# Performance work log

Measured on AMD Instinct MI355X. Metric: run time of the kernel, lower is better.

The kernel has to match this reference:

```python
import jax, jax.numpy as jnp
import numpy as np

B, S, H = 2, 2048, 1024
NH, HD = 16, 64
SCALE = HD ** -0.5


def setup_inputs() -> dict:
    key = jax.random.key(0)
    k1, k2, k3, k4 = jax.random.split(key, 4)
    hidden_states = jax.random.normal(k1, (B, S, H), dtype=jnp.float32)
    attention_mask = jax.random.randint(k2, (B, S), 0, 2, dtype=jnp.int32)
    # xavier-uniform-ish init scale
    w_qkv = jax.random.normal(k3, (3 * H, H), dtype=jnp.float32) * (2.0 / (H + 3 * H)) ** 0.5
    w_out = jax.random.normal(k4, (H, H), dtype=jnp.float32) * (1.0 / H) ** 0.5
    return {"hidden_states": hidden_states, "attention_mask": attention_mask,
            "w_qkv": w_qkv, "w_out": w_out}


def reference(hidden_states, attention_mask, w_qkv, w_out):
    b, s, _ = hidden_states.shape
    qkv = hidden_states @ w_qkv.T                      # [B,S,3H]
    q, k, v = jnp.split(qkv, 3, axis=-1)
    # [B,S,H] -> [B,NH,S,HD]
    reshape = lambda x: x.reshape(b, s, NH, HD).transpose(0, 2, 1, 3)
    q, k, v = reshape(q), reshape(k), reshape(v)
    scores = jnp.einsum('bhqd,bhkd->bhqk', q, k) * SCALE   # [B,NH,S,S]
    mask = attention_mask[:, None, None, :] == 0           # [B,1,1,S]
    scores = jnp.where(mask, -jnp.inf, scores)
    attn = jax.nn.softmax(scores, axis=-1)                 # dropout p: eval mode -> identity
    out = jnp.einsum('bhqk,bhkd->bhqd', attn, v)           # [B,NH,S,HD]
    out = out.transpose(0, 2, 1, 3).reshape(b, s, H)
    return out @ w_out.T
```

## Files before the change

### kernel.cpp

```cpp
#include <hip/hip_runtime.h>
#include <string.h>


typedef __bf16    bf16x8 __attribute__((ext_vector_type(8)));
typedef _Float16  f16x4  __attribute__((ext_vector_type(4)));
typedef _Float16  f16x2  __attribute__((ext_vector_type(2)));
typedef float     f32x4  __attribute__((ext_vector_type(4)));

#define NTOK   4096
#define HDIM   1024
#define SEQ    2048
#define NHEAD  16
#define F2SHIFT 4.0f
#define QSCALE  0.18033688f
#define LSTRIDE 68

__device__ __forceinline__ float bf2f(unsigned short u) {
    union { unsigned int i; float f; } x;
    x.i = ((unsigned int)u) << 16;
    return x.f;
}
__device__ __forceinline__ unsigned short f2bf(float f) {
    union { __bf16 h; unsigned short u; } x;
    x.h = (__bf16)f;
    return x.u;
}
__device__ __forceinline__ unsigned short f2h(float f) {
    union { _Float16 h; unsigned short u; } x;
    x.h = (_Float16)f;
    return x.u;
}
__device__ __forceinline__ f16x2 pkrtz(float a, float b) {
    union { __fp16 __attribute__((ext_vector_type(2))) i; f16x2 o; } x;
    x.i = __builtin_amdgcn_cvt_pkrtz(a, b);
    return x.o;
}

__device__ __forceinline__ int detect_f32(const unsigned short* hs) {
    unsigned int idx = (threadIdx.x & 63) * 4096u;
    float f = bf2f(hs[idx]);
    return __any(!(fabsf(f) < 1e4f));
}

typedef const __attribute__((address_space(1))) unsigned int* gptr_u32;
typedef __attribute__((address_space(3))) unsigned int* lptr_u32;

__device__ __forceinline__ void async16(const unsigned short* g, unsigned short* l) {
    __builtin_amdgcn_global_load_lds((gptr_u32)g, (lptr_u32)l, 16, 0, 0);
}

__global__ void convert3_kernel(const void* __restrict__ s0, const void* __restrict__ s1,
                                const void* __restrict__ s2, unsigned short* __restrict__ dst) {
    const int isf32 = detect_f32((const unsigned short*)s0);
    if (!isf32) return;
    int g = blockIdx.x * blockDim.x + threadIdx.x;
    const int stride = gridDim.x * blockDim.x;
    for (; g < 1048576; g += stride) {
        int i = g * 8;
        const void* src; int off;
        if (i < 4194304)      { src = s0; off = i; }
        else if (i < 7340032) { src = s1; off = i - 4194304; }
        else                  { src = s2; off = i - 7340032; }
        const float* s = (const float*)src + off;
        unsigned short o[8];
#pragma unroll
        for (int j = 0; j < 8; j++) o[j] = f2bf(s[j]);
        *(uint4*)(dst + i) = *(const uint4*)o;
    }
}

__global__ __launch_bounds__(256) void gemm_qkv(
    const unsigned short* __restrict__ Xc, const unsigned short* __restrict__ Wc,
    const unsigned short* __restrict__ Xraw, const unsigned short* __restrict__ Wraw,
    unsigned short* __restrict__ q_out, unsigned short* __restrict__ k_out,
    unsigned short* __restrict__ v_out) {
    const int K = 1024;
    __shared__ __align__(16) unsigned short Xs0[128 * 32];
    __shared__ __align__(16) unsigned short Xs1[128 * 32];
    __shared__ __align__(16) unsigned short Ws0[128 * 32];
    __shared__ __align__(16) unsigned short Ws1[128 * 32];

    const int isf32 = detect_f32(Xraw);
    const unsigned short* X = isf32 ? Xc : Xraw;
    const unsigned short* W = isf32 ? Wc : Wraw;

    const int t = threadIdx.x;
    const int w = t >> 6, lane = t & 63, quad = lane >> 4, lr = lane & 15;
    const int wrow = (w >> 1) * 64, wcol = (w & 1) * 64;

    const int hid = blockIdx.x;
    const int xcd = hid & 7, r = hid >> 3;
    const int by = xcd * 4 + r / 24;
    const int bx = r % 24;
    const int m0 = by * 128, n0 = bx * 128;
    const bool vblk = (n0 >= 2048);

    f32x4 acc[4][4];
#pragma unroll
    for (int mi = 0; mi < 4; mi++)
#pragma unroll
        for (int ni = 0; ni < 4; ni++) acc[mi][ni] = (f32x4){0.f, 0.f, 0.f, 0.f};

    const int srow = w * 32 + (lane >> 2);
    const int scol = (lane & 3) * 8;
    const unsigned short* xg = X + (size_t)(m0 + srow) * K + scol;
    const unsigned short* wg = W + (size_t)(n0 + srow) * K + scol;
    unsigned short* xl0 = &Xs0[w * 1024];
    unsigned short* xl1 = &Xs1[w * 1024];
    unsigned short* wl0 = &Ws0[w * 1024];
    unsigned short* wl1 = &Ws1[w * 1024];

    async16(xg, xl0);
    async16(xg + 16 * K, xl0 + 512);
    async16(wg, wl0);
    async16(wg + 16 * K, wl0 + 512);

#define QKV_COMPUTE(Xh, Wh)                                                            \
    {                                                                                  \
        bf16x8 af[4], bfr[4];                                                          \
        _Pragma("unroll")                                                              \
        for (int mi = 0; mi < 4; mi++)                                                 \
            af[mi] = *(const bf16x8*)&Xh[(wrow + mi * 16 + lr) * 32 + quad * 8];       \
        _Pragma("unroll")                                                              \
        for (int ni = 0; ni < 4; ni++)                                                 \
            bfr[ni] = *(const bf16x8*)&Wh[(wcol + ni * 16 + lr) * 32 + quad * 8];      \
        __builtin_amdgcn_s_setprio(1);                                                 \
        if (!vblk) {                                                                   \
            _Pragma("unroll")                                                          \
            for (int mi = 0; mi < 4; mi++)                                             \
                _Pragma("unroll")                                                      \
                for (int ni = 0; ni < 4; ni++)                                         \
                    acc[mi][ni] = __builtin_amdgcn_mfma_f32_16x16x32_bf16(             \
                        af[mi], bfr[ni], acc[mi][ni], 0, 0, 0);                        \
        } else {                                                                       \
            _Pragma("unroll")                                                          \
            for (int mi = 0; mi < 4; mi++)                                             \
                _Pragma("unroll")                                                      \
                for (int ni = 0; ni < 4; ni++)                                         \
                    acc[mi][ni] = __builtin_amdgcn_mfma_f32_16x16x32_bf16(             \
                        bfr[ni], af[mi], acc[mi][ni], 0, 0, 0);                        \
        }                                                                              \
        __builtin_amdgcn_s_setprio(0);                                                 \
    }

    for (int k0 = 0; k0 < K; k0 += 64) {
        __syncthreads();
        async16(xg + k0 + 32, xl1);
        async16(xg + k0 + 32 + 16 * K, xl1 + 512);
        async16(wg + k0 + 32, wl1);
        async16(wg + k0 + 32 + 16 * K, wl1 + 512);
        QKV_COMPUTE(Xs0, Ws0);

        __syncthreads();
        if (k0 + 64 < K) {
            async16(xg + k0 + 64, xl0);
            async16(xg + k0 + 64 + 16 * K, xl0 + 512);
            async16(wg + k0 + 64, wl0);
            async16(wg + k0 + 64 + 16 * K, wl0 + 512);
        }
        QKV_COMPUTE(Xs1, Ws1);
    }
#undef QKV_COMPUTE

    if (!vblk) {
#pragma unroll
        for (int mi = 0; mi < 4; mi++)
#pragma unroll
            for (int ni = 0; ni < 4; ni++)
#pragma unroll
                for (int rr = 0; rr < 4; rr++) {
                    int mrow = m0 + wrow + mi * 16 + quad * 4 + rr;
                    int j = n0 + wcol + ni * 16 + lr;
                    float val = acc[mi][ni][rr];
                    int which = j >> 10, rem = j & 1023;
                    int nh = rem >> 6, hd = rem & 63;
                    int b = mrow >> 11, s = mrow & 2047;
                    size_t dst = ((size_t)(b * NHEAD + nh) * SEQ + s) * 64 + hd;
                    if (which == 0) q_out[dst] = f2bf(val * QSCALE);
                    else            k_out[dst] = f2bf(val);
                }
    } else {
#pragma unroll
        for (int mi = 0; mi < 4; mi++)
#pragma unroll
            for (int ni = 0; ni < 4; ni++)
#pragma unroll
                for (int rr = 0; rr < 4; rr++) {
                    int n = n0 + wcol + ni * 16 + quad * 4 + rr;
                    int m = m0 + wrow + mi * 16 + lr;
                    float val = acc[mi][ni][rr];
                    int rem = n & 1023;
                    int nh = rem >> 6, hd = rem & 63;
                    int b = m >> 11, s = m & 2047;
                    size_t dst = ((size_t)(b * NHEAD + nh) * 64 + hd) * SEQ + s;
                    v_out[dst] = f2h(val);
                }
    }
}

__global__ __launch_bounds__(256) void gemm_out(
    const unsigned short* __restrict__ X, const unsigned short* __restrict__ Wc,
    const unsigned short* __restrict__ Wraw,
    void* __restrict__ d_out, const unsigned short* __restrict__ hs_raw) {
    const int K = 1024, N = 1024;
    __shared__ __align__(16) unsigned short Xs0[64 * 32];
    __shared__ __align__(16) unsigned short Xs1[64 * 32];
    __shared__ __align__(16) unsigned short Ws0[128 * 32];
    __shared__ __align__(16) unsigned short Ws1[128 * 32];

    const int isf32 = detect_f32(hs_raw);
    const unsigned short* W = isf32 ? Wc : Wraw;

    const int t = threadIdx.x;
    const int w = t >> 6, lane = t & 63, quad = lane >> 4, lr = lane & 15;
    const int wrow = (w >> 1) * 32, wcol = (w & 1) * 64;
    const int m0 = blockIdx.y * 64, n0 = blockIdx.x * 128;

    f32x4 acc[2][4];
#pragma unroll
    for (int mi = 0; mi < 2; mi++)
#pragma unroll
        for (int ni = 0; ni < 4; ni++) acc[mi][ni] = (f32x4){0.f, 0.f, 0.f, 0.f};

    const int sxrow = w * 16 + (lane >> 2);
    const int swrow = w * 32 + (lane >> 2);
    const int scol = (lane & 3) * 8;
    const unsigned short* xg = X + (size_t)(m0 + sxrow) * K + scol;
    const unsigned short* wg = W + (size_t)(n0 + swrow) * K + scol;
    unsigned short* xl0 = &Xs0[w * 512];
    unsigned short* xl1 = &Xs1[w * 512];
    unsigned short* wl0 = &Ws0[w * 1024];
    unsigned short* wl1 = &Ws1[w * 1024];

    async16(xg, xl0);
    async16(wg, wl0);
    async16(wg + 16 * K, wl0 + 512);

#define OUT_COMPUTE(Xh, Wh)                                                            \
    {                                                                                  \
        bf16x8 af[2], bfr[4];                                                          \
        _Pragma("unroll")                                                              \
        for (int mi = 0; mi < 2; mi++)                                                 \
            af[mi] = *(const bf16x8*)&Xh[(wrow + mi * 16 + lr) * 32 + quad * 8];       \
        _Pragma("unroll")                                                              \
        for (int ni = 0; ni < 4; ni++)                                                 \
            bfr[ni] = *(const bf16x8*)&Wh[(wcol + ni * 16 + lr) * 32 + quad * 8];      \
        __builtin_amdgcn_s_setprio(1);                                                 \
        _Pragma("unroll")                                                              \
        for (int mi = 0; mi < 2; mi++)                                                 \
            _Pragma("unroll")                                                          \
            for (int ni = 0; ni < 4; ni++)                                             \
                acc[mi][ni] = __builtin_amdgcn_mfma_f32_16x16x32_bf16(                 \
                    af[mi], bfr[ni], acc[mi][ni], 0, 0, 0);                            \
        __builtin_amdgcn_s_setprio(0);                                                 \
    }

    for (int k0 = 0; k0 < K; k0 += 64) {
        __syncthreads();
        async16(xg + k0 + 32, xl1);
        async16(wg + k0 + 32, wl1);
        async16(wg + k0 + 32 + 16 * K, wl1 + 512);
        OUT_COMPUTE(Xs0, Ws0);

        __syncthreads();
        if (k0 + 64 < K) {
            async16(xg + k0 + 64, xl0);
            async16(wg + k0 + 64, wl0);
            async16(wg + k0 + 64 + 16 * K, wl0 + 512);
        }
        OUT_COMPUTE(Xs1, Ws1);
    }
#undef OUT_COMPUTE

#pragma unroll
    for (int mi = 0; mi < 2; mi++)
#pragma unroll
        for (int ni = 0; ni < 4; ni++)
#pragma unroll
            for (int rr = 0; rr < 4; rr++) {
                int mrow = m0 + wrow + mi * 16 + quad * 4 + rr;
                int j = n0 + wcol + ni * 16 + lr;
                float val = acc[mi][ni][rr];
                size_t dst = (size_t)mrow * N + j;
                if (isf32) ((float*)d_out)[dst] = val;
                else ((unsigned short*)d_out)[dst] = f2bf(val);
            }
}

__global__ __launch_bounds__(256, 2) void flash_attn_v12(
    const unsigned short* __restrict__ q, const unsigned short* __restrict__ k,
    const unsigned short* __restrict__ vt, const int* __restrict__ mask,
    unsigned short* __restrict__ attn_out) {
    __shared__ __align__(16) unsigned short Ks[128 * LSTRIDE];
    __shared__ __align__(16) unsigned short Vt0[64 * LSTRIDE];
    __shared__ __align__(16) unsigned short Vt1[64 * LSTRIDE];
    __shared__ __align__(16) float Msk[136];

    const int t = threadIdx.x;
    const int w = t >> 6, lane = t & 63, quad = lane >> 4, lr = lane & 15;
    const int bh = blockIdx.x, b = bh >> 4, h = bh & 15;
    const int q0 = blockIdx.y * 128;

    const unsigned short* qb = q + (size_t)bh * SEQ * 64;
    const unsigned short* kb = k + (size_t)bh * SEQ * 64;
    const unsigned short* vtb = vt + (size_t)bh * 64 * SEQ;
    const int* mb = mask + b * SEQ;

    bf16x8 qf[2][2];
#pragma unroll
    for (int qg = 0; qg < 2; qg++) {
        const unsigned short* qrow = qb + (size_t)(q0 + w * 32 + qg * 16 + lr) * 64 + quad * 8;
        qf[qg][0] = *(const bf16x8*)qrow;
        qf[qg][1] = *(const bf16x8*)(qrow + 32);
    }

    f32x4 oacc[2][4];
#pragma unroll
    for (int qg = 0; qg < 2; qg++)
#pragma unroll
        for (int dt = 0; dt < 4; dt++) oacc[qg][dt] = (f32x4){0.f, 0.f, 0.f, 0.f};
    float l_st[2] = {0.f, 0.f};

    const int sr = t >> 2;
    const int sc = (t & 3) * 16;

    for (int kk0 = 0; kk0 < SEQ; kk0 += 128) {
        const uint4* kp0 = (const uint4*)(kb + (size_t)(kk0 + sr) * 64 + sc);
        const uint4* kp1 = (const uint4*)(kb + (size_t)(kk0 + 64 + sr) * 64 + sc);
        const uint4* vp0 = (const uint4*)(vtb + (size_t)sr * SEQ + kk0 + sc);
        const uint4* vp1 = (const uint4*)(vtb + (size_t)sr * SEQ + kk0 + 64 + sc);
        uint4 k0a = kp0[0], k0b = kp0[1];
        uint4 k1a = kp1[0], k1b = kp1[1];
        uint4 v0a = vp0[0], v0b = vp0[1];
        uint4 v1a = vp1[0], v1b = vp1[1];
        float mval = 0.f;
        if (t < 128) mval = (mb[kk0 + t] == 0) ? -1e30f : -F2SHIFT;

        __syncthreads();
        *(uint4*)&Ks[sr * LSTRIDE + sc] = k0a;
        *(uint4*)&Ks[sr * LSTRIDE + sc + 8] = k0b;
        *(uint4*)&Ks[(64 + sr) * LSTRIDE + sc] = k1a;
        *(uint4*)&Ks[(64 + sr) * LSTRIDE + sc + 8] = k1b;
        *(uint4*)&Vt0[sr * LSTRIDE + sc] = v0a;
        *(uint4*)&Vt0[sr * LSTRIDE + sc + 8] = v0b;
        *(uint4*)&Vt1[sr * LSTRIDE + sc] = v1a;
        *(uint4*)&Vt1[sr * LSTRIDE + sc + 8] = v1b;
        if (t < 128) Msk[t] = mval;
        __syncthreads();

        __builtin_amdgcn_s_setprio(1);
#pragma unroll
        for (int mt = 0; mt < 8; mt++) {
            bf16x8 a1h0 = *(bf16x8*)&Ks[(mt * 16 + lr) * LSTRIDE + quad * 8];
            bf16x8 a1h1 = *(bf16x8*)&Ks[(mt * 16 + lr) * LSTRIDE + 32 + quad * 8];
            const unsigned short* vb_ = (mt < 4) ? Vt0 : Vt1;
            const int mcol = (mt & 3) * 16;
            f16x4 a2[4];
#pragma unroll
            for (int dt = 0; dt < 4; dt++)
                a2[dt] = *(const f16x4*)&vb_[(dt * 16 + lr) * LSTRIDE + mcol + quad * 4];
            float4 mv = *(const float4*)&Msk[mt * 16 + quad * 4];
            f32x4 zi = (f32x4){mv.x, mv.y, mv.z, mv.w};

#pragma unroll
            for (int qg = 0; qg < 2; qg++) {
                f32x4 z = __builtin_amdgcn_mfma_f32_16x16x32_bf16(a1h0, qf[qg][0], zi, 0, 0, 0);
                z = __builtin_amdgcn_mfma_f32_16x16x32_bf16(a1h1, qf[qg][1], z, 0, 0, 0);
                float p0 = __builtin_amdgcn_exp2f(z[0]);
                float p1 = __builtin_amdgcn_exp2f(z[1]);
                float p2 = __builtin_amdgcn_exp2f(z[2]);
                float p3 = __builtin_amdgcn_exp2f(z[3]);
                l_st[qg] += (p0 + p1) + (p2 + p3);
                f16x2 ab = pkrtz(p0, p1);
                f16x2 cd = pkrtz(p2, p3);
                f16x4 b2;
                b2[0] = ab[0]; b2[1] = ab[1]; b2[2] = cd[0]; b2[3] = cd[1];
#pragma unroll
                for (int dt = 0; dt < 4; dt++)
                    oacc[qg][dt] = __builtin_amdgcn_mfma_f32_16x16x16f16(a2[dt], b2, oacc[qg][dt], 0, 0, 0);
            }
        }
        __builtin_amdgcn_s_setprio(0);
    }

    float inv[2];
#pragma unroll
    for (int qg = 0; qg < 2; qg++) {
        float s = l_st[qg];
        s += __shfl_xor(s, 16);
        s += __shfl_xor(s, 32);
        inv[qg] = 1.0f / s;
    }
#pragma unroll
    for (int qg = 0; qg < 2; qg++) {
        size_t tok = (size_t)(b * SEQ + q0 + w * 32 + qg * 16 + lr);
#pragma unroll
        for (int dt = 0; dt < 4; dt++)
#pragma unroll
            for (int rr = 0; rr < 4; rr++)
                attn_out[tok * HDIM + h * 64 + dt * 16 + quad * 4 + rr] =
                    f2bf(oacc[qg][dt][rr] * inv[qg]);
    }
}

extern "C" void kernel_launch(void* const* d_in, const int* in_sizes, int n_in,
                              void* d_out, int out_size, void* d_ws, size_t ws_size,
                              hipStream_t stream) {
    const void* hs_raw = d_in[0];
    const int* mask = (const int*)d_in[1];
    const void* wqkv_raw = d_in[2];
    const void* wout_raw = d_in[3];

    char* wsb = (char*)d_ws;
    unsigned short* hs_c = (unsigned short*)(wsb + 256);
    unsigned short* wqkv_c = hs_c + 4194304;
    unsigned short* wout_c = wqkv_c + 3145728;
    unsigned short* qw = wout_c + 1048576;
    unsigned short* kw = qw + 4194304;
    unsigned short* vtw = kw + 4194304;
    unsigned short* ao = vtw + 4194304;

    convert3_kernel<<<1024, 256, 0, stream>>>(hs_raw, wqkv_raw, wout_raw, hs_c);

    gemm_qkv<<<768, 256, 0, stream>>>(hs_c, wqkv_c,
                                      (const unsigned short*)hs_raw,
                                      (const unsigned short*)wqkv_raw,
                                      qw, kw, vtw);
    flash_attn_v12<<<dim3(32, 16), 256, 0, stream>>>(qw, kw, vtw, mask, ao);
    gemm_out<<<dim3(8, 64), 256, 0, stream>>>(ao, wout_c,
                                              (const unsigned short*)wout_raw, d_out,
                                              (const unsigned short*)hs_raw);
}
```

Measured before the change: 183.2 us.

## Triple-buffer QKV GEMM LDS tiles with vmcnt-based partial waits

Replaces the double-buffered K loop in the QKV projection GEMM with a three-stage LDS ring. Two tiles are prefetched ahead, and each step waits with s_waitcnt vmcnt(4) instead of a full __syncthreads drain, so the next tile's loads stay in flight during compute. This targets global-load latency exposed at each barrier. It costs 16KB more LDS per block, which may lower occupancy, and relies on the async copies counting against vmcnt.

```diff
diff --git a/kernel.cpp b/kernel.cpp
--- a/kernel.cpp
+++ b/kernel.cpp
@@ -77,8 +77,10 @@
     const int K = 1024;
     __shared__ __align__(16) unsigned short Xs0[128 * 32];
     __shared__ __align__(16) unsigned short Xs1[128 * 32];
+    __shared__ __align__(16) unsigned short Xs2[128 * 32];
     __shared__ __align__(16) unsigned short Ws0[128 * 32];
     __shared__ __align__(16) unsigned short Ws1[128 * 32];
+    __shared__ __align__(16) unsigned short Ws2[128 * 32];
 
     const int isf32 = detect_f32(Xraw);
     const unsigned short* X = isf32 ? Xc : Xraw;
@@ -107,13 +109,26 @@
     const unsigned short* wg = W + (size_t)(n0 + srow) * K + scol;
     unsigned short* xl0 = &Xs0[w * 1024];
     unsigned short* xl1 = &Xs1[w * 1024];
+    unsigned short* xl2 = &Xs2[w * 1024];
     unsigned short* wl0 = &Ws0[w * 1024];
     unsigned short* wl1 = &Ws1[w * 1024];
-
-    async16(xg, xl0);
-    async16(xg + 16 * K, xl0 + 512);
-    async16(wg, wl0);
-    async16(wg + 16 * K, wl0 + 512);
+    unsigned short* wl2 = &Ws2[w * 1024];
+
+#define QKV_STAGE(kk, xl, wl)                                   \
+    async16(xg + (kk), xl);                                     \
+    async16(xg + (kk) + 16 * K, xl + 512);                      \
+    async16(wg + (kk), wl);                                     \
+    async16(wg + (kk) + 16 * K, wl + 512);
+
+#define QKV_SYNC4()                                             \
+    asm volatile("s_waitcnt vmcnt(4)" ::: "memory");            \
+    __builtin_amdgcn_s_barrier();                               \
+    __builtin_amdgcn_sched_barrier(0);
+
+#define QKV_SYNC0()                                             \
+    asm volatile("s_waitcnt vmcnt(0)" ::: "memory");            \
+    __builtin_amdgcn_s_barrier();                               \
+    __builtin_amdgcn_sched_barrier(0);
 
 #define QKV_COMPUTE(Xh, Wh)                                                            \
     {                                                                                  \
@@ -143,24 +158,32 @@
         __builtin_amdgcn_s_setprio(0);                                                 \
     }
 
-    for (int k0 = 0; k0 < K; k0 += 64) {
-        __syncthreads();
-        async16(xg + k0 + 32, xl1);
-        async16(xg + k0 + 32 + 16 * K, xl1 + 512);
-        async16(wg + k0 + 32, wl1);
-        async16(wg + k0 + 32 + 16 * K, wl1 + 512);
+    QKV_STAGE(0, xl0, wl0);
+    QKV_STAGE(32, xl1, wl1);
+
+    int k = 0;
+#pragma unroll 1
+    for (int g = 0; g < 10; g++) {
+        QKV_SYNC4();
+        QKV_STAGE(k + 64, xl2, wl2);
         QKV_COMPUTE(Xs0, Ws0);
-
-        __syncthreads();
-        if (k0 + 64 < K) {
-            async16(xg + k0 + 64, xl0);
-            async16(xg + k0 + 64 + 16 * K, xl0 + 512);
-            async16(wg + k0 + 64, wl0);
-            async16(wg + k0 + 64 + 16 * K, wl0 + 512);
-        }
+        QKV_SYNC4();
+        QKV_STAGE(k + 96, xl0, wl0);
         QKV_COMPUTE(Xs1, Ws1);
-    }
+        QKV_SYNC4();
+        QKV_STAGE(k + 128, xl1, wl1);
+        QKV_COMPUTE(Xs2, Ws2);
+        k += 96;
+    }
+    QKV_SYNC4();
+    QKV_COMPUTE(Xs0, Ws0);
+    QKV_SYNC0();
+    QKV_COMPUTE(Xs1, Ws1);
+
 #undef QKV_COMPUTE
+#undef QKV_STAGE
+#undef QKV_SYNC4
+#undef QKV_SYNC0
 
     if (!vblk) {
 #pragma unroll
```

New measurement: 193.5 us. 1.06x slower.
